# Performance work log

Measured on AMD Instinct MI355X. Metric: run time of the kernel, lower is better.

The kernel has to match this reference:

```python
import jax, jax.numpy as jnp
import numpy as np

B = 524288  # batch size (number of ODE state samples)
D = 32      # state dimension (in_dim == out_dim forced by x.mm(weight) shape)


def setup_inputs() -> dict:
    key = jax.random.key(0)
    k1, k2, k3 = jax.random.split(key, 3)
    x = jax.random.normal(k1, (B, D), dtype=jnp.float32)
    # LinearODELayer weight, init uniform(-0.1, 0.1); used as x @ W_lin directly.
    W_lin = jax.random.uniform(k2, (D, D), dtype=jnp.float32, minval=-0.1, maxval=0.1)
    # NonLinearODELayer weight [D, D, D], init uniform(-0.001, 0.001).
    W_nl = jax.random.uniform(k3, (D, D, D), dtype=jnp.float32, minval=-0.001, maxval=0.001)
    return {"x": x, "W_lin": W_lin, "W_nl": W_nl}


def reference(x, W_lin, W_nl):
    # LinearODELayer: x.mm(weight) -> [B, D]
    lin = x @ W_lin
    # NonLinearODELayer: the matmul -> matmul(x.t()) -> permute -> diagonal -> t()
    # chain is exactly the batched bilinear form out[b, o] = x[b] @ W_nl[o] @ x[b].
    nl = jnp.einsum("bi,oij,bj->bo", x, W_nl, x)
    return lin + nl
```

## Files before the change

### kernel.cpp

```cpp
#include <hip/hip_runtime.h>


typedef __attribute__((ext_vector_type(8))) __bf16 bf16x8;
typedef __attribute__((ext_vector_type(4))) float floatx4;
typedef __attribute__((ext_vector_type(2))) float floatx2;

#define NB     524288
#define NTILES (NB / 16)
#define GRID   1024
#define ITERS  (NTILES / GRID)
#define XROW   36
#define XBUF   (16 * XROW)
#define REDW   544
#define REDB   (4 * REDW)

__global__ __launch_bounds__(256, 4)
void nnode_kernel(const float* __restrict__ x, const float* __restrict__ Wlin,
                  const float* __restrict__ Wnl, float* __restrict__ out) {
    __shared__ __align__(16) float xs[2][XBUF];
    __shared__ __align__(16) float red[2][REDB];

    const int tid  = threadIdx.x;
    const int wave = tid >> 6;
    const int lane = tid & 63;
    const int q    = lane >> 4;
    const int col  = lane & 15;

    int eoffs[5], woffs[5];
    bf16x8 bW[5][2];
    #pragma unroll
    for (int kl = 0; kl < 5; ++kl) {
        const int t  = wave * 5 + kl;
        const int p  = t >> 1, h = t & 1;
        const int pa = (p < 4) ? 0 : ((p < 7) ? 1 : ((p < 9) ? 2 : 3));
        const int pb = p - ((p < 4) ? 0 : ((p < 7) ? 3 : ((p < 9) ? 5 : 6)));
        eoffs[kl] = 8 * pa + 4 * h;
        woffs[kl] = 8 * pb;
        const bool diag = (pa == pb);
        const int  i1   = eoffs[kl] + q;
        #pragma unroll
        for (int tt = 0; tt < 2; ++tt) {
            const float* base = Wnl + (size_t)(col + 16 * tt) * 1024;
            floatx4 v0 = *(const floatx4*)(base + i1 * 32 + woffs[kl]);
            floatx4 v1 = *(const floatx4*)(base + i1 * 32 + woffs[kl] + 4);
            if (!diag) {
                #pragma unroll
                for (int j = 0; j < 4; ++j) {
                    v0[j] += base[(size_t)(woffs[kl] + j) * 32 + i1];
                    v1[j] += base[(size_t)(woffs[kl] + 4 + j) * 32 + i1];
                }
            }
            bf16x8 f;
            #pragma unroll
            for (int j = 0; j < 4; ++j) { f[j] = (__bf16)v0[j]; f[j + 4] = (__bf16)v1[j]; }
            bW[kl][tt] = f;
        }
    }

    bf16x8 bl0, bl1;
    #pragma unroll
    for (int j = 0; j < 8; ++j) {
        bl0[j] = (__bf16)(0.25f * Wlin[(q * 8 + j) * 32 + col]);
        bl1[j] = (__bf16)(0.25f * Wlin[(q * 8 + j) * 32 + col + 16]);
    }

    const int srow  = tid >> 4;
    const int scol2 = (tid & 15) * 2;

    {
        floatx2 v = *(const floatx2*)(x + (size_t)blockIdx.x * 512 + tid * 2);
        *(floatx2*)&xs[0][srow * XROW + scol2] = v;
    }
    __syncthreads();

    for (int it = 0; it < ITERS; ++it) {
        const int b0  = (blockIdx.x + it * GRID) << 4;
        const int cur = it & 1;

        floatx2 pre;
        if (it < ITERS - 1)
            pre = *(const floatx2*)(x + ((size_t)b0 + GRID * 16) * 32 + tid * 2);

        const float* xr = &xs[cur][col * XROW];
        floatx4 acc0 = {0.f, 0.f, 0.f, 0.f};
        floatx4 acc1 = {0.f, 0.f, 0.f, 0.f};

        {
            floatx4 a0 = *(const floatx4*)(xr + q * 8);
            floatx4 a1 = *(const floatx4*)(xr + q * 8 + 4);
            bf16x8 af;
            #pragma unroll
            for (int j = 0; j < 4; ++j) { af[j] = (__bf16)a0[j]; af[j + 4] = (__bf16)a1[j]; }
            acc0 = __builtin_amdgcn_mfma_f32_16x16x32_bf16(af, bl0, acc0, 0, 0, 0);
            acc1 = __builtin_amdgcn_mfma_f32_16x16x32_bf16(af, bl1, acc1, 0, 0, 0);
        }

        #pragma unroll
        for (int kl = 0; kl < 5; ++kl) {
            const float sc = xr[eoffs[kl] + q];
            floatx4 w0 = *(const floatx4*)(xr + woffs[kl]);
            floatx4 w1 = *(const floatx4*)(xr + woffs[kl] + 4);
            bf16x8 af;
            #pragma unroll
            for (int j = 0; j < 4; ++j) {
                af[j]     = (__bf16)(sc * w0[j]);
                af[j + 4] = (__bf16)(sc * w1[j]);
            }
            acc0 = __builtin_amdgcn_mfma_f32_16x16x32_bf16(af, bW[kl][0], acc0, 0, 0, 0);
            acc1 = __builtin_amdgcn_mfma_f32_16x16x32_bf16(af, bW[kl][1], acc1, 0, 0, 0);
        }

        float* rp = red[cur] + wave * REDW;
        #pragma unroll
        for (int r = 0; r < 4; ++r) {
            rp[(q * 4 + r) * 34 + col]      = acc0[r];
            rp[(q * 4 + r) * 34 + col + 16] = acc1[r];
        }
        if (it < ITERS - 1)
            *(floatx2*)&xs[cur ^ 1][srow * XROW + scol2] = pre;
        __syncthreads();

        const float* rb = red[cur];
        floatx2 sum = *(const floatx2*)(rb + srow * 34 + scol2);
        #pragma unroll
        for (int w = 1; w < 4; ++w) {
            floatx2 pp = *(const floatx2*)(rb + w * REDW + srow * 34 + scol2);
            sum.x += pp.x; sum.y += pp.y;
        }
        *(floatx2*)(out + (size_t)b0 * 32 + tid * 2) = sum;
    }
}

extern "C" void kernel_launch(void* const* d_in, const int* in_sizes, int n_in,
                              void* d_out, int out_size, void* d_ws, size_t ws_size,
                              hipStream_t stream) {
    const float* x    = (const float*)d_in[0];
    const float* Wlin = (const float*)d_in[1];
    const float* Wnl  = (const float*)d_in[2];
    float* out        = (float*)d_out;
    nnode_kernel<<<dim3(GRID), dim3(256), 0, stream>>>(x, Wlin, Wnl, out);
}
```

Before: 171.1 us.

## Process 32-row chunks per iteration with swizzled LDS and vectorized reduction

After: 185.9 us. 8.7% more time.

```diff
diff --git a/kernel.cpp b/kernel.cpp
--- a/kernel.cpp
+++ b/kernel.cpp
@@ -3,22 +3,21 @@
 
 typedef __attribute__((ext_vector_type(8))) __bf16 bf16x8;
 typedef __attribute__((ext_vector_type(4))) float floatx4;
-typedef __attribute__((ext_vector_type(2))) float floatx2;
 
 #define NB     524288
-#define NTILES (NB / 16)
+#define NCHUNK (NB / 32)
 #define GRID   1024
-#define ITERS  (NTILES / GRID)
-#define XROW   36
-#define XBUF   (16 * XROW)
-#define REDW   544
-#define REDB   (4 * REDW)
+#define ITERS  (NCHUNK / GRID)
+
+__device__ __forceinline__ int XW(int r, int e) {
+    return r * 32 + ((((e >> 2) ^ (r & 7)) << 2) | (e & 3));
+}
 
 __global__ __launch_bounds__(256, 4)
 void nnode_kernel(const float* __restrict__ x, const float* __restrict__ Wlin,
                   const float* __restrict__ Wnl, float* __restrict__ out) {
-    __shared__ __align__(16) float xs[2][XBUF];
-    __shared__ __align__(16) float red[2][REDB];
+    __shared__ __align__(16) float xs[2][1024];
+    __shared__ __align__(16) float red[2][2][2048];
 
     const int tid  = threadIdx.x;
     const int wave = tid >> 6;
@@ -64,70 +63,85 @@
         bl1[j] = (__bf16)(0.25f * Wlin[(q * 8 + j) * 32 + col + 16]);
     }
 
-    const int srow  = tid >> 4;
-    const int scol2 = (tid & 15) * 2;
+    const int sword = (tid >> 3) * 32 + (((tid & 7) ^ ((tid >> 3) & 7)) << 2);
+    const int pofs  = ((q + (col >> 1)) & 3) << 2;
+    const int rt  = tid >> 7;
+    const int rc  = tid & 31;
+    const int rqd = (tid >> 5) & 3;
+    const int rp4 = ((rqd + (rc >> 1)) & 3) << 2;
 
     {
-        floatx2 v = *(const floatx2*)(x + (size_t)blockIdx.x * 512 + tid * 2);
-        *(floatx2*)&xs[0][srow * XROW + scol2] = v;
+        floatx4 v = *(const floatx4*)(x + (size_t)blockIdx.x * 1024 + tid * 4);
+        *(floatx4*)&xs[0][sword] = v;
     }
     __syncthreads();
 
     for (int it = 0; it < ITERS; ++it) {
-        const int b0  = (blockIdx.x + it * GRID) << 4;
-        const int cur = it & 1;
+        const int chunk = blockIdx.x + it * GRID;
+        const int cur   = it & 1;
 
-        floatx2 pre;
+        floatx4 pre;
         if (it < ITERS - 1)
-            pre = *(const floatx2*)(x + ((size_t)b0 + GRID * 16) * 32 + tid * 2);
+            pre = *(const floatx4*)(x + (size_t)(chunk + GRID) * 1024 + tid * 4);
 
-        const float* xr = &xs[cur][col * XROW];
-        floatx4 acc0 = {0.f, 0.f, 0.f, 0.f};
-        floatx4 acc1 = {0.f, 0.f, 0.f, 0.f};
+        const float* xb = xs[cur];
+        floatx4 acc0[2] = {{0.f,0.f,0.f,0.f},{0.f,0.f,0.f,0.f}};
+        floatx4 acc1[2] = {{0.f,0.f,0.f,0.f},{0.f,0.f,0.f,0.f}};
 
-        {
-            floatx4 a0 = *(const floatx4*)(xr + q * 8);
-            floatx4 a1 = *(const floatx4*)(xr + q * 8 + 4);
-            bf16x8 af;
+        #pragma unroll
+        for (int t = 0; t < 2; ++t) {
+            const int r = t * 16 + col;
+
+            {
+                floatx4 a0 = *(const floatx4*)(xb + XW(r, q * 8));
+                floatx4 a1 = *(const floatx4*)(xb + XW(r, q * 8 + 4));
+                bf16x8 af;
+                #pragma unroll
+                for (int j = 0; j < 4; ++j) { af[j] = (__bf16)a0[j]; af[j + 4] = (__bf16)a1[j]; }
+                acc0[t] = __builtin_amdgcn_mfma_f32_16x16x32_bf16(af, bl0, acc0[t], 0, 0, 0);
+                acc1[t] = __builtin_amdgcn_mfma_f32_16x16x32_bf16(af, bl1, acc1[t], 0, 0, 0);
+            }
+
             #pragma unroll
-            for (int j = 0; j < 4; ++j) { af[j] = (__bf16)a0[j]; af[j + 4] = (__bf16)a1[j]; }
-            acc0 = __builtin_amdgcn_mfma_f32_16x16x32_bf16(af, bl0, acc0, 0, 0, 0);
-            acc1 = __builtin_amdgcn_mfma_f32_16x16x32_bf16(af, bl1, acc1, 0, 0, 0);
+            for (int kl = 0; kl < 5; ++kl) {
+                const float sc = xb[XW(r, eoffs[kl] + q)];
+                floatx4 w0 = *(const floatx4*)(xb + XW(r, woffs[kl]));
+                floatx4 w1 = *(const floatx4*)(xb + XW(r, woffs[kl] + 4));
+                bf16x8 af;
+                #pragma unroll
+                for (int j = 0; j < 4; ++j) {
+                    af[j]     = (__bf16)(sc * w0[j]);
+                    af[j + 4] = (__bf16)(sc * w1[j]);
+                }
+                acc0[t] = __builtin_amdgcn_mfma_f32_16x16x32_bf16(af, bW[kl][0], acc0[t], 0, 0, 0);
+                acc1[t] = __builtin_amdgcn_mfma_f32_16x16x32_bf16(af, bW[kl][1], acc1[t], 0, 0, 0);
+            }
         }
 
         #pragma unroll
-        for (int kl = 0; kl < 5; ++kl) {
-            const float sc = xr[eoffs[kl] + q];
-            floatx4 w0 = *(const floatx4*)(xr + woffs[kl]);
-            floatx4 w1 = *(const floatx4*)(xr + woffs[kl] + 4);
-            bf16x8 af;
-            #pragma unroll
-            for (int j = 0; j < 4; ++j) {
-                af[j]     = (__bf16)(sc * w0[j]);
-                af[j + 4] = (__bf16)(sc * w1[j]);
-            }
-            acc0 = __builtin_amdgcn_mfma_f32_16x16x32_bf16(af, bW[kl][0], acc0, 0, 0, 0);
-            acc1 = __builtin_amdgcn_mfma_f32_16x16x32_bf16(af, bW[kl][1], acc1, 0, 0, 0);
-        }
-
-        float* rp = red[cur] + wave * REDW;
-        #pragma unroll
-        for (int r = 0; r < 4; ++r) {
-            rp[(q * 4 + r) * 34 + col]      = acc0[r];
-            rp[(q * 4 + r) * 34 + col + 16] = acc1[r];
+        for (int t = 0; t < 2; ++t) {
+            float* rp = red[cur][t] + wave * 512;
+            *(floatx4*)(rp + col * 16 + pofs)        = acc0[t];
+            *(floatx4*)(rp + (col + 16) * 16 + pofs) = acc1[t];
         }
         if (it < ITERS - 1)
-            *(floatx2*)&xs[cur ^ 1][srow * XROW + scol2] = pre;
+            *(floatx4*)&xs[cur ^ 1][sword] = pre;
         __syncthreads();
 
-        const float* rb = red[cur];
-        floatx2 sum = *(const floatx2*)(rb + srow * 34 + scol2);
-        #pragma unroll
-        for (int w = 1; w < 4; ++w) {
-            floatx2 pp = *(const floatx2*)(rb + w * REDW + srow * 34 + scol2);
-            sum.x += pp.x; sum.y += pp.y;
+        {
+            const float* rb = red[cur][rt];
+            floatx4 s = *(const floatx4*)(rb + rc * 16 + rp4);
+            #pragma unroll
+            for (int w = 1; w < 4; ++w) {
+                floatx4 p = *(const floatx4*)(rb + w * 512 + rc * 16 + rp4);
+                s.x += p.x; s.y += p.y; s.z += p.z; s.w += p.w;
+            }
+            float* op = out + ((size_t)chunk * 32 + rt * 16 + rqd * 4) * 32 + rc;
+            op[0]  = s.x;
+            op[32] = s.y;
+            op[64] = s.z;
+            op[96] = s.w;
         }
-        *(floatx2*)(out + (size_t)b0 * 32 + tid * 2) = sum;
     }
 }
 
```

## Swizzle x tile in LDS and specialize per-wave bilinear steps with register-resident rows

Applied to the files above, without the earlier changes.

Result: faster. 162.7 us (-4.9%).

```diff
diff --git a/kernel.cpp b/kernel.cpp
--- a/kernel.cpp
+++ b/kernel.cpp
@@ -9,15 +9,24 @@
 #define NTILES (NB / 16)
 #define GRID   1024
 #define ITERS  (NTILES / GRID)
-#define XROW   36
-#define XBUF   (16 * XROW)
 #define REDW   544
 #define REDB   (4 * REDW)
+
+__device__ __forceinline__ int XW(int r, int e) {
+    return r * 32 + ((((e >> 2) ^ (r & 7)) << 2) | (e & 3));
+}
+
+__device__ __forceinline__ bf16x8 pack8(floatx4 a, floatx4 b) {
+    bf16x8 f;
+    #pragma unroll
+    for (int j = 0; j < 4; ++j) { f[j] = (__bf16)a[j]; f[j + 4] = (__bf16)b[j]; }
+    return f;
+}
 
 __global__ __launch_bounds__(256, 4)
 void nnode_kernel(const float* __restrict__ x, const float* __restrict__ Wlin,
                   const float* __restrict__ Wnl, float* __restrict__ out) {
-    __shared__ __align__(16) float xs[2][XBUF];
+    __shared__ __align__(16) float xs[2][512];
     __shared__ __align__(16) float red[2][REDB];
 
     const int tid  = threadIdx.x;
@@ -26,7 +35,6 @@
     const int q    = lane >> 4;
     const int col  = lane & 15;
 
-    int eoffs[5], woffs[5];
     bf16x8 bW[5][2];
     #pragma unroll
     for (int kl = 0; kl < 5; ++kl) {
@@ -34,26 +42,20 @@
         const int p  = t >> 1, h = t & 1;
         const int pa = (p < 4) ? 0 : ((p < 7) ? 1 : ((p < 9) ? 2 : 3));
         const int pb = p - ((p < 4) ? 0 : ((p < 7) ? 3 : ((p < 9) ? 5 : 6)));
-        eoffs[kl] = 8 * pa + 4 * h;
-        woffs[kl] = 8 * pb;
-        const bool diag = (pa == pb);
-        const int  i1   = eoffs[kl] + q;
+        const int i1 = 8 * pa + 4 * h + q;
         #pragma unroll
         for (int tt = 0; tt < 2; ++tt) {
             const float* base = Wnl + (size_t)(col + 16 * tt) * 1024;
-            floatx4 v0 = *(const floatx4*)(base + i1 * 32 + woffs[kl]);
-            floatx4 v1 = *(const floatx4*)(base + i1 * 32 + woffs[kl] + 4);
-            if (!diag) {
+            floatx4 v0 = *(const floatx4*)(base + i1 * 32 + 8 * pb);
+            floatx4 v1 = *(const floatx4*)(base + i1 * 32 + 8 * pb + 4);
+            if (pa != pb) {
                 #pragma unroll
                 for (int j = 0; j < 4; ++j) {
-                    v0[j] += base[(size_t)(woffs[kl] + j) * 32 + i1];
-                    v1[j] += base[(size_t)(woffs[kl] + 4 + j) * 32 + i1];
+                    v0[j] += base[(size_t)(8 * pb + j) * 32 + i1];
+                    v1[j] += base[(size_t)(8 * pb + 4 + j) * 32 + i1];
                 }
             }
-            bf16x8 f;
-            #pragma unroll
-            for (int j = 0; j < 4; ++j) { f[j] = (__bf16)v0[j]; f[j + 4] = (__bf16)v1[j]; }
-            bW[kl][tt] = f;
+            bW[kl][tt] = pack8(v0, v1);
         }
     }
 
@@ -64,51 +66,65 @@
         bl1[j] = (__bf16)(0.25f * Wlin[(q * 8 + j) * 32 + col + 16]);
     }
 
+    const bool q1 = (q & 1) != 0;
+    const bool q2 = (q & 2) != 0;
+
     const int srow  = tid >> 4;
     const int scol2 = (tid & 15) * 2;
 
     {
         floatx2 v = *(const floatx2*)(x + (size_t)blockIdx.x * 512 + tid * 2);
-        *(floatx2*)&xs[0][srow * XROW + scol2] = v;
+        *(floatx2*)&xs[0][XW(srow, scol2)] = v;
     }
     __syncthreads();
 
-    for (int it = 0; it < ITERS; ++it) {
-        const int b0  = (blockIdx.x + it * GRID) << 4;
+    int it = 0;
+    for (int tile = blockIdx.x; tile < NTILES; tile += GRID, ++it) {
+        const int b0  = tile << 4;
         const int cur = it & 1;
 
         floatx2 pre;
         if (it < ITERS - 1)
             pre = *(const floatx2*)(x + ((size_t)b0 + GRID * 16) * 32 + tid * 2);
 
-        const float* xr = &xs[cur][col * XROW];
+        const float* xb = xs[cur];
+        floatx4 X[8];
+        #pragma unroll
+        for (int j = 0; j < 8; ++j)
+            X[j] = *(const floatx4*)&xb[XW(col, 4 * j)];
+
         floatx4 acc0 = {0.f, 0.f, 0.f, 0.f};
         floatx4 acc1 = {0.f, 0.f, 0.f, 0.f};
 
+        #define SELQ(V) (q2 ? (q1 ? (V)[3] : (V)[2]) : (q1 ? (V)[1] : (V)[0]))
+
         {
-            floatx4 a0 = *(const floatx4*)(xr + q * 8);
-            floatx4 a1 = *(const floatx4*)(xr + q * 8 + 4);
-            bf16x8 af;
-            #pragma unroll
-            for (int j = 0; j < 4; ++j) { af[j] = (__bf16)a0[j]; af[j + 4] = (__bf16)a1[j]; }
+            floatx4 la0 = q2 ? (q1 ? X[6] : X[4]) : (q1 ? X[2] : X[0]);
+            floatx4 la1 = q2 ? (q1 ? X[7] : X[5]) : (q1 ? X[3] : X[1]);
+            bf16x8 af = pack8(la0, la1);
             acc0 = __builtin_amdgcn_mfma_f32_16x16x32_bf16(af, bl0, acc0, 0, 0, 0);
             acc1 = __builtin_amdgcn_mfma_f32_16x16x32_bf16(af, bl1, acc1, 0, 0, 0);
         }
 
-        #pragma unroll
-        for (int kl = 0; kl < 5; ++kl) {
-            const float sc = xr[eoffs[kl] + q];
-            floatx4 w0 = *(const floatx4*)(xr + woffs[kl]);
-            floatx4 w1 = *(const floatx4*)(xr + woffs[kl] + 4);
-            bf16x8 af;
-            #pragma unroll
-            for (int j = 0; j < 4; ++j) {
-                af[j]     = (__bf16)(sc * w0[j]);
-                af[j + 4] = (__bf16)(sc * w1[j]);
-            }
-            acc0 = __builtin_amdgcn_mfma_f32_16x16x32_bf16(af, bW[kl][0], acc0, 0, 0, 0);
-            acc1 = __builtin_amdgcn_mfma_f32_16x16x32_bf16(af, bW[kl][1], acc1, 0, 0, 0);
+        #define STEP(A, B, H, KL) {                                             \
+            const float sc = SELQ(X[2 * (A) + (H)]);                            \
+            floatx4 p0 = sc * X[2 * (B)];                                       \
+            floatx4 p1 = sc * X[2 * (B) + 1];                                   \
+            bf16x8 af = pack8(p0, p1);                                          \
+            acc0 = __builtin_amdgcn_mfma_f32_16x16x32_bf16(af, bW[KL][0], acc0, 0, 0, 0); \
+            acc1 = __builtin_amdgcn_mfma_f32_16x16x32_bf16(af, bW[KL][1], acc1, 0, 0, 0); }
+
+        if (wave == 0) {
+            STEP(0,0,0,0) STEP(0,0,1,1) STEP(0,1,0,2) STEP(0,1,1,3) STEP(0,2,0,4)
+        } else if (wave == 1) {
+            STEP(0,2,1,0) STEP(0,3,0,1) STEP(0,3,1,2) STEP(1,1,0,3) STEP(1,1,1,4)
+        } else if (wave == 2) {
+            STEP(1,2,0,0) STEP(1,2,1,1) STEP(1,3,0,2) STEP(1,3,1,3) STEP(2,2,0,4)
+        } else {
+            STEP(2,2,1,0) STEP(2,3,0,1) STEP(2,3,1,2) STEP(3,3,0,3) STEP(3,3,1,4)
         }
+        #undef STEP
+        #undef SELQ
 
         float* rp = red[cur] + wave * REDW;
         #pragma unroll
@@ -117,7 +133,7 @@
             rp[(q * 4 + r) * 34 + col + 16] = acc1[r];
         }
         if (it < ITERS - 1)
-            *(floatx2*)&xs[cur ^ 1][srow * XROW + scol2] = pre;
+            *(floatx2*)&xs[cur ^ 1][XW(srow, scol2)] = pre;
         __syncthreads();
 
         const float* rb = red[cur];
```
